# Kernel tuning notes

Measured on AMD Instinct MI355X. Metric: run time of the kernel, lower is better.

## Reference

```python
import jax, jax.numpy as jnp
import numpy as np

B, T, F, H, S = 4096, 200, 76, 128, 17


def setup_inputs() -> dict:
    key = jax.random.key(0)
    ks = jax.random.split(key, 10)
    kf = 1.0 / np.sqrt(H)
    return {
        "x": jax.random.normal(ks[0], (B, T, F), dtype=jnp.float32),
        "static": jax.random.normal(ks[1], (B, S), dtype=jnp.float32),
        "h0": jax.random.normal(ks[2], (B, H), dtype=jnp.float32),
        "c0": jax.random.normal(ks[3], (B, H), dtype=jnp.float32),
        "W_ih": jax.random.uniform(ks[4], (4 * H, F), jnp.float32, -kf, kf),
        "W_hh": jax.random.uniform(ks[5], (4 * H, H), jnp.float32, -kf, kf),
        "b_ih": jax.random.uniform(ks[6], (4 * H,), jnp.float32, -kf, kf),
        "b_hh": jax.random.uniform(ks[7], (4 * H,), jnp.float32, -kf, kf),
        "W_lin": jax.random.uniform(ks[8], (1, H + S), jnp.float32, -kf, kf),
        "b_lin": jax.random.uniform(ks[9], (1,), jnp.float32, -kf, kf),
    }


def reference(x, static, h0, c0, W_ih, W_hh, b_ih, b_hh, W_lin, b_lin):
    # Precompute input projections for all timesteps in one big GEMM: [B,T,4H]
    x_proj = jnp.einsum("btf,gf->btg", x, W_ih) + b_ih
    xs = jnp.swapaxes(x_proj, 0, 1)  # time-major [T, B, 4H]

    def step(carry, xp):
        h, c = carry
        gates = xp + h @ W_hh.T + b_hh  # [B, 4H]
        i, f, g, o = jnp.split(gates, 4, axis=-1)
        i, f, o = jax.nn.sigmoid(i), jax.nn.sigmoid(f), jax.nn.sigmoid(o)
        c = f * c + i * jnp.tanh(g)
        h = o * jnp.tanh(c)
        return (h, c), None

    (h, c), _ = jax.lax.scan(step, (h0, c0), xs)
    full = jnp.concatenate([h, static], axis=1)  # [B, H+S]
    predictions = full @ W_lin.T + b_lin  # [B, 1]
    return predictions
```

## Files before the change

kernel.cpp:

```cpp
#include <hip/hip_runtime.h>
#include <hip/hip_bf16.h>

#define B_TOT   4096
#define T_LEN   200
#define F_IN    76
#define H_DIM   128
#define S_DIM   17
#define BLK_B   16
#define NTHREADS 512
#define NT_CHUNK 8
#define NCHUNK  (T_LEN / NT_CHUNK)
#define XPITCH  96
#define HPITCH  136
#define ROW_F4  ((NT_CHUNK * F_IN) / 4)
#define PF_N    5

static_assert(NCHUNK * NT_CHUNK == T_LEN, "chunking must cover T exactly");

using f32x4 = __attribute__((ext_vector_type(4))) float;
using s16x8 = __attribute__((ext_vector_type(8))) short;

#if __has_builtin(__builtin_amdgcn_exp2f)
#define EXP2(v) __builtin_amdgcn_exp2f(v)
#else
#define EXP2(v) exp2f(v)
#endif
#if __has_builtin(__builtin_amdgcn_rcpf)
#define RCP(v) __builtin_amdgcn_rcpf(v)
#else
#define RCP(v) (1.0f / (v))
#endif

__device__ __forceinline__ short f2bf(float f) {
    union { float f; unsigned u; } v; v.f = f;
    unsigned r = v.u + 0x7FFFu + ((v.u >> 16) & 1u);
    return (short)(r >> 16);
}
__device__ __forceinline__ float bf2f(short s) {
    union { unsigned u; float f; } v;
    v.u = ((unsigned)(unsigned short)s) << 16;
    return v.f;
}
__device__ __forceinline__ unsigned cvt_pk_bf16(float lo, float hi) {
    unsigned r;
    asm("v_cvt_pk_bf16_f32 %0, %1, %2" : "=v"(r) : "v"(lo), "v"(hi));
    return r;
}

#define LDS_BARRIER() asm volatile("s_waitcnt lgkmcnt(0)\n\ts_barrier" ::: "memory")

__global__ __launch_bounds__(NTHREADS, 2) void lstm_fused(
    const float* __restrict__ x,    const float* __restrict__ stat,
    const float* __restrict__ h0,   const float* __restrict__ c0,
    const float* __restrict__ W_ih, const float* __restrict__ W_hh,
    const float* __restrict__ b_ih, const float* __restrict__ b_hh,
    const float* __restrict__ W_lin, const float* __restrict__ b_lin,
    float* __restrict__ out)
{
    __shared__ __align__(16) short xbuf[2][NT_CHUNK][BLK_B][XPITCH];
    __shared__ __align__(16) short hbuf[2][BLK_B][HPITCH];

    const int tid  = threadIdx.x;
    const int lane = tid & 63;
    const int wave = tid >> 6;
    const int lrow = lane & 15;
    const int lk8  = (lane >> 4) << 3;
    const int r0   = (lane >> 4) << 2;
    const int b0   = blockIdx.x * BLK_B;
    const int hb   = wave << 4;

    const float C1 = 1.44269504088896f;
    const float gs[4] = { -C1, -C1, -2.0f * C1, -C1 };

    s16x8 wih[4][3], whh[4][4];
    f32x4 biasf[4];
#pragma unroll
    for (int nt = 0; nt < 4; ++nt) {
        const int col = nt * H_DIM + hb + lrow;
        const float s = gs[nt];
#pragma unroll
        for (int kt = 0; kt < 3; ++kt) {
            s16x8 f;
#pragma unroll
            for (int j = 0; j < 8; ++j) {
                int k = kt * 32 + lk8 + j;
                float v = (k < F_IN) ? W_ih[col * F_IN + k] * s : 0.0f;
                f[j] = f2bf(v);
            }
            wih[nt][kt] = f;
        }
#pragma unroll
        for (int kt = 0; kt < 4; ++kt) {
            s16x8 f;
#pragma unroll
            for (int j = 0; j < 8; ++j) {
                int k = kt * 32 + lk8 + j;
                f[j] = f2bf(W_hh[col * H_DIM + k] * s);
            }
            whh[nt][kt] = f;
        }
        float bv = (b_ih[col] + b_hh[col]) * s;
        biasf[nt] = (f32x4){ bv, bv, bv, bv };
    }

    float c[4];
#pragma unroll
    for (int r = 0; r < 4; ++r)
        c[r] = c0[(b0 + r0 + r) * H_DIM + hb + lrow];

    for (int i = tid; i < BLK_B * H_DIM; i += NTHREADS) {
        int row = i >> 7, cc = i & 127;
        hbuf[0][row][cc] = f2bf(h0[(b0 + row) * H_DIM + cc]);
    }
    for (int i = tid; i < 2 * NT_CHUNK * BLK_B * (XPITCH - F_IN); i += NTHREADS) {
        int rem = i;
        int f   = rem % (XPITCH - F_IN); rem /= (XPITCH - F_IN);
        int row = rem % BLK_B;           rem /= BLK_B;
        int tt  = rem % NT_CHUNK;        rem /= NT_CHUNK;
        xbuf[rem][tt][row][F_IN + f] = 0;
    }

    const int prow = tid >> 5;
    const int pidx = tid & 31;
    const float* psrc = x + (size_t)(b0 + prow) * (T_LEN * F_IN) + pidx * 4;
    int ldsoff[PF_N];
#pragma unroll
    for (int i = 0; i < PF_N; ++i) {
        int s4 = pidx + 32 * i;
        int q  = 4 * s4;
        int tp = (q * 863) >> 16;
        int f0 = q - 76 * tp;
        ldsoff[i] = (tp * BLK_B + prow) * XPITCH + f0;
    }

    f32x4 pf[PF_N];
    auto issue = [&](int ch) {
        const float* p = psrc + (size_t)ch * (NT_CHUNK * F_IN);
#pragma unroll
        for (int i = 0; i < PF_N; ++i)
            if (i < PF_N - 1 || pidx < ROW_F4 - 4 * 32)
                pf[i] = *(const f32x4*)(p + i * 128);
    };
    auto commit = [&](int buf) {
        short* xb0 = &xbuf[buf][0][0][0];
#pragma unroll
        for (int i = 0; i < PF_N; ++i)
            if (i < PF_N - 1 || pidx < ROW_F4 - 4 * 32) {
                unsigned lo = cvt_pk_bf16(pf[i].x, pf[i].y);
                unsigned hi = cvt_pk_bf16(pf[i].z, pf[i].w);
                unsigned long long v = ((unsigned long long)hi << 32) | lo;
                *(unsigned long long*)(xb0 + ldsoff[i]) = v;
            }
    };

    issue(0);
    commit(0);
    __syncthreads();

    s16x8 axr[3];
    f32x4 xa[4];
    auto load_ax = [&](int buf, int tt) {
#pragma unroll
        for (int kt = 0; kt < 3; ++kt)
            axr[kt] = *(const s16x8*)&xbuf[buf][tt][lrow][kt * 32 + lk8];
    };

#define REBUILD(NT)                                                              \
    xa[NT] = __builtin_amdgcn_mfma_f32_16x16x32_bf16(axr[2], wih[NT][2],         \
             __builtin_amdgcn_mfma_f32_16x16x32_bf16(axr[1], wih[NT][1],         \
             __builtin_amdgcn_mfma_f32_16x16x32_bf16(axr[0], wih[NT][0],         \
             biasf[NT], 0, 0, 0), 0, 0, 0), 0, 0, 0)

#define NONLIN(R)                                                                \
    {   float A  = EXP2(acc[0][R]);                                              \
        float Bv = EXP2(acc[1][R]);                                              \
        float E  = EXP2(acc[2][R]);                                              \
        float Dv = EXP2(acc[3][R]);                                              \
        float p1 = 1.f + A, p2 = 1.f + Bv, p3 = 1.f + E;                         \
        float q13 = p1 * p3;                                                     \
        float num = fmaf(c[R], q13, (1.f - E) * p2);                             \
        float cn  = num * RCP(q13 * p2);                                         \
        c[R] = cn;                                                               \
        float Ec  = EXP2(fminf(cn * (-2.f * C1), 80.f));                         \
        hv[R] = (1.f - Ec) * RCP((1.f + Dv) * (1.f + Ec)); }

    load_ax(0, 0);
    REBUILD(0); REBUILD(1); REBUILD(2); REBUILD(3);

#define STEP(CUR, TT)                                                            \
    {                                                                            \
        s16x8 ah[4];                                                             \
        _Pragma("unroll")                                                        \
        for (int kt = 0; kt < 4; ++kt)                                           \
            ah[kt] = *(const s16x8*)&hbuf[CUR][lrow][kt * 32 + lk8];             \
        if ((TT) < NT_CHUNK - 1) load_ax(xc, (TT) + 1);                          \
        f32x4 acc[4];                                                            \
        _Pragma("unroll")                                                        \
        for (int nt = 0; nt < 4; ++nt) {                                         \
            f32x4 t = __builtin_amdgcn_mfma_f32_16x16x32_bf16(ah[0], whh[nt][0], xa[nt], 0, 0, 0); \
            t = __builtin_amdgcn_mfma_f32_16x16x32_bf16(ah[1], whh[nt][1], t, 0, 0, 0); \
            t = __builtin_amdgcn_mfma_f32_16x16x32_bf16(ah[2], whh[nt][2], t, 0, 0, 0); \
            t = __builtin_amdgcn_mfma_f32_16x16x32_bf16(ah[3], whh[nt][3], t, 0, 0, 0); \
            acc[nt] = t;                                                         \
        }                                                                        \
        if ((TT) == 0 && ch + 1 < NCHUNK) issue(ch + 1);                         \
        float hv[4];                                                             \
        unsigned short* hp = (unsigned short*)&hbuf[(CUR) ^ 1][r0][hb + lrow];   \
        NONLIN(0);                                                               \
        if ((TT) < NT_CHUNK - 1) { REBUILD(0); }                                 \
        NONLIN(1);                                                               \
        {   unsigned q01 = cvt_pk_bf16(hv[0], hv[1]);                            \
            hp[0 * HPITCH] = (unsigned short)q01;                                \
            hp[1 * HPITCH] = (unsigned short)(q01 >> 16); }                      \
        if ((TT) < NT_CHUNK - 1) { REBUILD(1); }                                 \
        NONLIN(2);                                                               \
        if ((TT) < NT_CHUNK - 1) { REBUILD(2); }                                 \
        NONLIN(3);                                                               \
        {   unsigned q23 = cvt_pk_bf16(hv[2], hv[3]);                            \
            hp[2 * HPITCH] = (unsigned short)q23;                                \
            hp[3 * HPITCH] = (unsigned short)(q23 >> 16); }                      \
        if ((TT) < NT_CHUNK - 1) { REBUILD(3); }                                 \
        if ((TT) == NT_CHUNK - 1 && ch + 1 < NCHUNK) commit(xc ^ 1);             \
        LDS_BARRIER();                                                           \
    }

#pragma unroll 1
    for (int ch = 0; ch < NCHUNK; ++ch) {
        const int xc = ch & 1;
        STEP(0, 0)
        STEP(1, 1)
        STEP(0, 2)
        STEP(1, 3)
        STEP(0, 4)
        STEP(1, 5)
        STEP(0, 6)
        STEP(1, 7)
        if (ch + 1 < NCHUNK) {
            load_ax(xc ^ 1, 0);
            REBUILD(0); REBUILD(1); REBUILD(2); REBUILD(3);
        }
    }
#undef STEP
#undef NONLIN
#undef REBUILD

    if (tid < BLK_B) {
        const int row = tid;
        float a = b_lin[0];
        for (int k = 0; k < H_DIM; ++k)
            a += bf2f(hbuf[0][row][k]) * W_lin[k];
        for (int s = 0; s < S_DIM; ++s)
            a += stat[(b0 + row) * S_DIM + s] * W_lin[H_DIM + s];
        out[b0 + row] = a;
    }
}

extern "C" void kernel_launch(void* const* d_in, const int* in_sizes, int n_in,
                              void* d_out, int out_size, void* d_ws, size_t ws_size,
                              hipStream_t stream) {
    const float* xx   = (const float*)d_in[0];
    const float* st   = (const float*)d_in[1];
    const float* h0   = (const float*)d_in[2];
    const float* c0   = (const float*)d_in[3];
    const float* Wih  = (const float*)d_in[4];
    const float* Whh  = (const float*)d_in[5];
    const float* bih  = (const float*)d_in[6];
    const float* bhh  = (const float*)d_in[7];
    const float* Wlin = (const float*)d_in[8];
    const float* blin = (const float*)d_in[9];
    float* o = (float*)d_out;

    lstm_fused<<<B_TOT / BLK_B, NTHREADS, 0, stream>>>(
        xx, st, h0, c0, Wih, Whh, bih, bhh, Wlin, blin, o);
}
```

Baseline: 205.6 us.

## Stagger even/odd waves' MFMA and nonlinearity phases with double-buffered input projections

Splits the per-step schedule so even waves run the recurrent MFMA then the nonlinearity then the next input-projection rebuild, while odd waves rebuild first. The goal is for one wave's transcendental math to overlap with another wave's matrix work on the same SIMD. The input projection accumulators are double-buffered (xa0/xa1) so the next step's projection can be computed before the current one is consumed. MFMA blocks are raised with s_setprio, and the x LDS pitch changes from 96 to 104, likely to reduce bank conflicts. The extra live accumulators raise register pressure and could lower occupancy.

```diff
diff --git a/kernel.cpp b/kernel.cpp
--- a/kernel.cpp
+++ b/kernel.cpp
@@ -10,7 +10,7 @@
 #define NTHREADS 512
 #define NT_CHUNK 8
 #define NCHUNK  (T_LEN / NT_CHUNK)
-#define XPITCH  96
+#define XPITCH  104
 #define HPITCH  136
 #define ROW_F4  ((NT_CHUNK * F_IN) / 4)
 #define PF_N    5
@@ -158,20 +158,42 @@
     __syncthreads();
 
     s16x8 axr[3];
-    f32x4 xa[4];
+    f32x4 xa0[4], xa1[4];
     auto load_ax = [&](int buf, int tt) {
 #pragma unroll
         for (int kt = 0; kt < 3; ++kt)
             axr[kt] = *(const s16x8*)&xbuf[buf][tt][lrow][kt * 32 + lk8];
     };
 
-#define REBUILD(NT)                                                              \
-    xa[NT] = __builtin_amdgcn_mfma_f32_16x16x32_bf16(axr[2], wih[NT][2],         \
-             __builtin_amdgcn_mfma_f32_16x16x32_bf16(axr[1], wih[NT][1],         \
-             __builtin_amdgcn_mfma_f32_16x16x32_bf16(axr[0], wih[NT][0],         \
-             biasf[NT], 0, 0, 0), 0, 0, 0), 0, 0, 0)
-
-#define NONLIN(R)                                                                \
+#define REBUILD_ALL(XA)                                                          \
+    {   __builtin_amdgcn_s_setprio(1);                                           \
+        _Pragma("unroll")                                                        \
+        for (int nt = 0; nt < 4; ++nt) {                                         \
+            f32x4 t = __builtin_amdgcn_mfma_f32_16x16x32_bf16(axr[0], wih[nt][0], biasf[nt], 0, 0, 0); \
+            t = __builtin_amdgcn_mfma_f32_16x16x32_bf16(axr[1], wih[nt][1], t, 0, 0, 0); \
+            t = __builtin_amdgcn_mfma_f32_16x16x32_bf16(axr[2], wih[nt][2], t, 0, 0, 0); \
+            XA[nt] = t;                                                          \
+        }                                                                        \
+        __builtin_amdgcn_s_setprio(0); }
+
+#define LOAD_AH(CUR)                                                             \
+    _Pragma("unroll")                                                            \
+    for (int kt = 0; kt < 4; ++kt)                                               \
+        ah[kt] = *(const s16x8*)&hbuf[CUR][lrow][kt * 32 + lk8];
+
+#define HMFMA(XA)                                                                \
+    {   __builtin_amdgcn_s_setprio(1);                                           \
+        _Pragma("unroll")                                                        \
+        for (int nt = 0; nt < 4; ++nt) {                                         \
+            f32x4 t = __builtin_amdgcn_mfma_f32_16x16x32_bf16(ah[0], whh[nt][0], XA[nt], 0, 0, 0); \
+            t = __builtin_amdgcn_mfma_f32_16x16x32_bf16(ah[1], whh[nt][1], t, 0, 0, 0); \
+            t = __builtin_amdgcn_mfma_f32_16x16x32_bf16(ah[2], whh[nt][2], t, 0, 0, 0); \
+            t = __builtin_amdgcn_mfma_f32_16x16x32_bf16(ah[3], whh[nt][3], t, 0, 0, 0); \
+            acc[nt] = t;                                                         \
+        }                                                                        \
+        __builtin_amdgcn_s_setprio(0); }
+
+#define NONLIN1(R)                                                               \
     {   float A  = EXP2(acc[0][R]);                                              \
         float Bv = EXP2(acc[1][R]);                                              \
         float E  = EXP2(acc[2][R]);                                              \
@@ -184,42 +206,38 @@
         float Ec  = EXP2(fminf(cn * (-2.f * C1), 80.f));                         \
         hv[R] = (1.f - Ec) * RCP((1.f + Dv) * (1.f + Ec)); }
 
+#define NONLIN_ALL(CUR)                                                          \
+    {   float hv[4];                                                             \
+        NONLIN1(0); NONLIN1(1); NONLIN1(2); NONLIN1(3);                          \
+        unsigned q01 = cvt_pk_bf16(hv[0], hv[1]);                                \
+        unsigned q23 = cvt_pk_bf16(hv[2], hv[3]);                                \
+        unsigned short* hp = (unsigned short*)&hbuf[(CUR) ^ 1][r0][hb + lrow];   \
+        hp[0 * HPITCH] = (unsigned short)q01;                                    \
+        hp[1 * HPITCH] = (unsigned short)(q01 >> 16);                            \
+        hp[2 * HPITCH] = (unsigned short)q23;                                    \
+        hp[3 * HPITCH] = (unsigned short)(q23 >> 16); }
+
     load_ax(0, 0);
-    REBUILD(0); REBUILD(1); REBUILD(2); REBUILD(3);
-
-#define STEP(CUR, TT)                                                            \
+    REBUILD_ALL(xa0)
+
+#define STEP(CUR, TT, XA_C, XA_N)                                                \
     {                                                                            \
         s16x8 ah[4];                                                             \
-        _Pragma("unroll")                                                        \
-        for (int kt = 0; kt < 4; ++kt)                                           \
-            ah[kt] = *(const s16x8*)&hbuf[CUR][lrow][kt * 32 + lk8];             \
-        if ((TT) < NT_CHUNK - 1) load_ax(xc, (TT) + 1);                          \
         f32x4 acc[4];                                                            \
-        _Pragma("unroll")                                                        \
-        for (int nt = 0; nt < 4; ++nt) {                                         \
-            f32x4 t = __builtin_amdgcn_mfma_f32_16x16x32_bf16(ah[0], whh[nt][0], xa[nt], 0, 0, 0); \
-            t = __builtin_amdgcn_mfma_f32_16x16x32_bf16(ah[1], whh[nt][1], t, 0, 0, 0); \
-            t = __builtin_amdgcn_mfma_f32_16x16x32_bf16(ah[2], whh[nt][2], t, 0, 0, 0); \
-            t = __builtin_amdgcn_mfma_f32_16x16x32_bf16(ah[3], whh[nt][3], t, 0, 0, 0); \
-            acc[nt] = t;                                                         \
+        if (!(wave & 1)) {                                                       \
+            LOAD_AH(CUR)                                                         \
+            HMFMA(XA_C)                                                          \
+            if ((TT) == 0 && ch + 1 < NCHUNK) issue(ch + 1);                     \
+            if ((TT) < NT_CHUNK - 1) load_ax(xc, (TT) + 1);                      \
+            NONLIN_ALL(CUR)                                                      \
+            if ((TT) < NT_CHUNK - 1) REBUILD_ALL(XA_N)                           \
+        } else {                                                                 \
+            if ((TT) < NT_CHUNK - 1) { load_ax(xc, (TT) + 1); REBUILD_ALL(XA_N) } \
+            LOAD_AH(CUR)                                                         \
+            HMFMA(XA_C)                                                          \
+            if ((TT) == 0 && ch + 1 < NCHUNK) issue(ch + 1);                     \
+            NONLIN_ALL(CUR)                                                      \
         }                                                                        \
-        if ((TT) == 0 && ch + 1 < NCHUNK) issue(ch + 1);                         \
-        float hv[4];                                                             \
-        unsigned short* hp = (unsigned short*)&hbuf[(CUR) ^ 1][r0][hb + lrow];   \
-        NONLIN(0);                                                               \
-        if ((TT) < NT_CHUNK - 1) { REBUILD(0); }                                 \
-        NONLIN(1);                                                               \
-        {   unsigned q01 = cvt_pk_bf16(hv[0], hv[1]);                            \
-            hp[0 * HPITCH] = (unsigned short)q01;                                \
-            hp[1 * HPITCH] = (unsigned short)(q01 >> 16); }                      \
-        if ((TT) < NT_CHUNK - 1) { REBUILD(1); }                                 \
-        NONLIN(2);                                                               \
-        if ((TT) < NT_CHUNK - 1) { REBUILD(2); }                                 \
-        NONLIN(3);                                                               \
-        {   unsigned q23 = cvt_pk_bf16(hv[2], hv[3]);                            \
-            hp[2 * HPITCH] = (unsigned short)q23;                                \
-            hp[3 * HPITCH] = (unsigned short)(q23 >> 16); }                      \
-        if ((TT) < NT_CHUNK - 1) { REBUILD(3); }                                 \
         if ((TT) == NT_CHUNK - 1 && ch + 1 < NCHUNK) commit(xc ^ 1);             \
         LDS_BARRIER();                                                           \
     }
@@ -227,22 +245,25 @@
 #pragma unroll 1
     for (int ch = 0; ch < NCHUNK; ++ch) {
         const int xc = ch & 1;
-        STEP(0, 0)
-        STEP(1, 1)
-        STEP(0, 2)
-        STEP(1, 3)
-        STEP(0, 4)
-        STEP(1, 5)
-        STEP(0, 6)
-        STEP(1, 7)
+        STEP(0, 0, xa0, xa1)
+        STEP(1, 1, xa1, xa0)
+        STEP(0, 2, xa0, xa1)
+        STEP(1, 3, xa1, xa0)
+        STEP(0, 4, xa0, xa1)
+        STEP(1, 5, xa1, xa0)
+        STEP(0, 6, xa0, xa1)
+        STEP(1, 7, xa1, xa0)
         if (ch + 1 < NCHUNK) {
             load_ax(xc ^ 1, 0);
-            REBUILD(0); REBUILD(1); REBUILD(2); REBUILD(3);
+            REBUILD_ALL(xa0)
         }
     }
 #undef STEP
-#undef NONLIN
-#undef REBUILD
+#undef NONLIN_ALL
+#undef NONLIN1
+#undef HMFMA
+#undef LOAD_AH
+#undef REBUILD_ALL
 
     if (tid < BLK_B) {
         const int row = tid;
```

Measured after the change: 251.4 us. 1.22x slower.
